# Performance work log

Measured on AMD Instinct MI355X. Metric: run time of the kernel, lower is better.

## Reference

```python
import jax, jax.numpy as jnp
import numpy as np

EMB = 1024
HEADS = 16
HEAD_DIM = EMB // HEADS
MASK_VAL = -10000.0


def setup_inputs() -> dict:
    key = jax.random.key(0)
    ks = jax.random.split(key, 5)
    B, S = 4, 2048
    x = jax.random.normal(ks[0], (B, S, EMB), dtype=jnp.float32)
    scale = 1.0 / np.sqrt(EMB)
    w_qkv = jax.random.normal(ks[1], (EMB, 3 * EMB), dtype=jnp.float32) * scale
    b_qkv = jnp.zeros((3 * EMB,), dtype=jnp.float32)
    w_fc = jax.random.normal(ks[2], (EMB, EMB), dtype=jnp.float32) * scale
    b_fc = jnp.zeros((EMB,), dtype=jnp.float32)
    return {"x": x, "w_qkv": w_qkv, "b_qkv": b_qkv, "w_fc": w_fc, "b_fc": b_fc}


def reference(x, w_qkv, b_qkv, w_fc, b_fc):
    B, S, _ = x.shape
    qkv = x @ w_qkv + b_qkv                      # (B, S, 3*EMB)
    q, k, v = jnp.split(qkv, 3, axis=-1)
    # split heads: (B, S, EMB) -> (B, H, S, Dh)
    def sh(t):
        return t.reshape(B, S, HEADS, HEAD_DIM).transpose(0, 2, 1, 3)
    q, k, v = sh(q), sh(k), sh(v)
    scores = jnp.einsum('bhqd,bhkd->bhqk', q, k) / np.sqrt(HEAD_DIM)
    causal = jnp.tril(jnp.ones((S, S), dtype=bool))[None, None]
    scores = jnp.where(causal, scores, jnp.float32(MASK_VAL))
    probs = jax.nn.softmax(scores, axis=-1)
    out = jnp.einsum('bhqk,bhkd->bhqd', probs, v)
    out = out.transpose(0, 2, 1, 3).reshape(B, S, EMB)  # merge heads
    return out @ w_fc + b_fc
```

## Files before the change

kernel.cpp:

```cpp
#include <hip/hip_runtime.h>
#include <hip/hip_bf16.h>
#include <cstdint>

#define BF16 __hip_bfloat16

typedef __attribute__((ext_vector_type(8))) short bhalf8;
typedef __attribute__((ext_vector_type(4))) float floatx4;

#define MFMA16(a, b, c) __builtin_amdgcn_mfma_f32_16x16x32_bf16((a), (b), (c), 0, 0, 0)

#define MASKV (-30000.0f)
#define QSCALE 0.18033688011112042f

__device__ __forceinline__ bhalf8 cvt8(const float* p) {
  const float4 f0 = *(const float4*)p;
  const float4 f1 = *(const float4*)(p + 4);
  union { bhalf8 v; ushort u[8]; } r;
  const float t[8] = {f0.x, f0.y, f0.z, f0.w, f1.x, f1.y, f1.z, f1.w};
#pragma unroll
  for (int i = 0; i < 8; ++i) {
    BF16 h = __float2bfloat16(t[i]);
    r.u[i] = *(const ushort*)&h;
  }
  return r.v;
}

__global__ void cvt_f32_bf16(const float* __restrict__ in, BF16* __restrict__ out) {
  const size_t i = ((size_t)blockIdx.x * 256 + threadIdx.x) * 8;
  *(bhalf8*)(out + i) = cvt8(in + i);
}

__global__ void transpose_cvt(const float* __restrict__ in, ushort* __restrict__ out,
                              int R, int C) {
  __shared__ ushort t[32][33];
  const int c0 = blockIdx.x * 32, r0 = blockIdx.y * 32;
  const int tx = threadIdx.x, ty = threadIdx.y;
#pragma unroll
  for (int j = 0; j < 32; j += 8) {
    BF16 h = __float2bfloat16(in[(size_t)(r0 + ty + j) * C + c0 + tx]);
    t[ty + j][tx] = *(const ushort*)&h;
  }
  __syncthreads();
#pragma unroll
  for (int j = 0; j < 32; j += 8)
    out[(size_t)(c0 + ty + j) * R + r0 + tx] = t[tx][ty + j];
}

template <int MODE>
__global__ __launch_bounds__(256, 2) void gemm_bt(
    const BF16* __restrict__ A, const BF16* __restrict__ Bt, const float* __restrict__ bias,
    void* __restrict__ C0v, BF16* __restrict__ C1, BF16* __restrict__ C2,
    int Md, int Nd, int Kd) {
  __shared__ __align__(16) BF16 As[128 * 64];
  __shared__ __align__(16) BF16 Bs[128 * 64];

  const int tid = threadIdx.x;
  const int w = tid >> 6, lane = tid & 63;
  const int lm = lane & 15, quad = lane >> 4;
  const int wm = (w >> 1) * 64, wn = (w & 1) * 64;
  const int tile_m = blockIdx.y * 128, tile_n = blockIdx.x * 128;

  floatx4 acc[4][4];
#pragma unroll
  for (int i = 0; i < 4; ++i)
#pragma unroll
    for (int j = 0; j < 4; ++j) acc[i][j] = (floatx4){0.f, 0.f, 0.f, 0.f};

  int srow[4], sgs[4], sslot[4];
#pragma unroll
  for (int j = 0; j < 4; ++j) {
    const int slot = (j * 4 + w) * 64 + lane;
    sslot[j] = slot;
    srow[j] = slot >> 3;
    sgs[j] = ((slot & 7) - (slot >> 3)) & 7;
  }

  bhalf8 va[4], vb[4], nva[4], nvb[4];
#pragma unroll
  for (int j = 0; j < 4; ++j) {
    va[j] = *(const bhalf8*)(A + (size_t)(tile_m + srow[j]) * Kd + sgs[j] * 8);
    vb[j] = *(const bhalf8*)(Bt + (size_t)(tile_n + srow[j]) * Kd + sgs[j] * 8);
  }

  for (int k0 = 0; k0 < Kd; k0 += 64) {
    __syncthreads();
#pragma unroll
    for (int j = 0; j < 4; ++j) {
      *(bhalf8*)(As + sslot[j] * 8) = va[j];
      *(bhalf8*)(Bs + sslot[j] * 8) = vb[j];
    }
    __syncthreads();

    if (k0 + 64 < Kd) {
      const int k1 = k0 + 64;
#pragma unroll
      for (int j = 0; j < 4; ++j) {
        nva[j] = *(const bhalf8*)(A + (size_t)(tile_m + srow[j]) * Kd + k1 + sgs[j] * 8);
        nvb[j] = *(const bhalf8*)(Bt + (size_t)(tile_n + srow[j]) * Kd + k1 + sgs[j] * 8);
      }
    }

#pragma unroll
    for (int s = 0; s < 2; ++s) {
      bhalf8 af[4], bfr[4];
#pragma unroll
      for (int mt = 0; mt < 4; ++mt) {
        const int r = wm + mt * 16 + lm;
        const int g = ((s * 4 + quad) + r) & 7;
        af[mt] = *(const bhalf8*)(As + r * 64 + g * 8);
      }
#pragma unroll
      for (int nt = 0; nt < 4; ++nt) {
        const int r = wn + nt * 16 + lm;
        const int g = ((s * 4 + quad) + r) & 7;
        bfr[nt] = *(const bhalf8*)(Bs + r * 64 + g * 8);
      }
#pragma unroll
      for (int mt = 0; mt < 4; ++mt)
#pragma unroll
        for (int nt = 0; nt < 4; ++nt)
          acc[mt][nt] = MFMA16(af[mt], bfr[nt], acc[mt][nt]);
    }
#pragma unroll
    for (int j = 0; j < 4; ++j) { va[j] = nva[j]; vb[j] = nvb[j]; }
  }

#pragma unroll
  for (int nt = 0; nt < 4; ++nt) {
    const int n = tile_n + wn + nt * 16 + lm;
    const float bv = bias[n];
#pragma unroll
    for (int mt = 0; mt < 4; ++mt) {
      const int m0 = tile_m + wm + mt * 16 + quad * 4;
      floatx4 v = acc[mt][nt];
      if (MODE == 0) {
        float* C0f = (float*)C0v;
#pragma unroll
        for (int r = 0; r < 4; ++r)
          C0f[(size_t)(m0 + r) * Nd + n] = v[r] + bv;
      } else {
        const int which = n >> 10;
        const int h = (n >> 6) & 15;
        const int d = n & 63;
        if (which == 2) {
          const int b = m0 >> 11, s0 = m0 & 2047;
          union { ushort4 u4; ushort u[4]; } pk;
#pragma unroll
          for (int r = 0; r < 4; ++r) {
            BF16 hv = __float2bfloat16(v[r] + bv);
            pk.u[r] = *(const ushort*)&hv;
          }
          *(ushort4*)(C2 + ((size_t)((b * 16 + h) * 64 + d)) * 2048 + s0) = pk.u4;
        } else {
          BF16* dst = (which == 0) ? (BF16*)C0v : C1;
          const float sc = (which == 0) ? QSCALE : 1.0f;
#pragma unroll
          for (int r = 0; r < 4; ++r) {
            const int m = m0 + r, b = m >> 11, si = m & 2047;
            dst[((size_t)(b * 16 + h) * 2048 + si) * 64 + d] =
                __float2bfloat16((v[r] + bv) * sc);
          }
        }
      }
    }
  }
}

__global__ __launch_bounds__(256, 2) void flash_attn(
    const BF16* __restrict__ Q, const BF16* __restrict__ Kmat,
    const BF16* __restrict__ VT, BF16* __restrict__ O) {
  __shared__ __align__(16) BF16 Ps[4][4][16 * 64];

  const int tid = threadIdx.x;
  const int w = tid >> 6, lane = tid & 63;
  const int lm = lane & 15, quad = lane >> 4;

  const int bid = blockIdx.x;
  const int xcd = bid & 7;
  const int li = bid >> 3;
  const int bh = xcd * 8 + (li >> 3);
  const int x = li & 7;

  const int qt = (w == 0) ? x : (w == 1) ? (15 - x) : (w == 2) ? (16 + x) : (31 - x);
  const int qb0 = qt * 64;
  const size_t bh_off = (size_t)bh * (2048 * 64);

  bhalf8 aq[4][2];
#pragma unroll
  for (int s2 = 0; s2 < 4; ++s2) {
    const BF16* qp = Q + bh_off + (size_t)(qb0 + s2 * 16 + lm) * 64 + quad * 8;
    aq[s2][0] = *(const bhalf8*)qp;
    aq[s2][1] = *(const bhalf8*)(qp + 32);
  }

  floatx4 oacc[4][4];
  float m_i[4], l_i[4];
#pragma unroll
  for (int s2 = 0; s2 < 4; ++s2) {
    m_i[s2] = MASKV;
    l_i[s2] = 0.f;
#pragma unroll
    for (int i = 0; i < 4; ++i) oacc[s2][i] = (floatx4){0.f, 0.f, 0.f, 0.f};
  }

  for (int kt = 0; kt <= qt; ++kt) {
    const int k0 = kt * 64;

    bhalf8 ak[4][2], av[4][2];
#pragma unroll
    for (int nt = 0; nt < 4; ++nt) {
      const BF16* kp = Kmat + bh_off + (size_t)(k0 + nt * 16 + lm) * 64 + quad * 8;
      ak[nt][0] = *(const bhalf8*)kp;
      ak[nt][1] = *(const bhalf8*)(kp + 32);
      const BF16* vp = VT + bh_off + (size_t)(nt * 16 + lm) * 2048 + k0 + quad * 8;
      av[nt][0] = *(const bhalf8*)vp;
      av[nt][1] = *(const bhalf8*)(vp + 32);
    }

#pragma unroll
    for (int s2 = 0; s2 < 4; ++s2) {
      const int qb = qb0 + s2 * 16;
      if (k0 > qb + 15) continue;

      floatx4 st[4];
#pragma unroll
      for (int nt = 0; nt < 4; ++nt) {
        floatx4 z = (floatx4){0.f, 0.f, 0.f, 0.f};
        z = MFMA16(ak[nt][0], aq[s2][0], z);
        z = MFMA16(ak[nt][1], aq[s2][1], z);
        st[nt] = z;
      }

      if (k0 + 63 > qb) {
#pragma unroll
        for (int nt = 0; nt < 4; ++nt)
#pragma unroll
          for (int r = 0; r < 4; ++r)
            if ((k0 + nt * 16 + quad * 4 + r) > (qb + lm)) st[nt][r] = MASKV;
      }

      float mx = MASKV;
#pragma unroll
      for (int nt = 0; nt < 4; ++nt)
#pragma unroll
        for (int r = 0; r < 4; ++r) mx = fmaxf(mx, st[nt][r]);
      mx = fmaxf(mx, __shfl_xor(mx, 16, 64));
      mx = fmaxf(mx, __shfl_xor(mx, 32, 64));

      if (!__all(mx <= m_i[s2] + 8.0f)) {
        const float mnew = fmaxf(m_i[s2], mx);
        const float alpha = __builtin_amdgcn_exp2f(m_i[s2] - mnew);
        m_i[s2] = mnew;
        l_i[s2] *= alpha;
#pragma unroll
        for (int dn = 0; dn < 4; ++dn) oacc[s2][dn] *= alpha;
      }

      float rs = 0.f;
#pragma unroll
      for (int nt = 0; nt < 4; ++nt)
#pragma unroll
        for (int r = 0; r < 4; ++r) {
          const float p = __builtin_amdgcn_exp2f(st[nt][r] - m_i[s2]);
          st[nt][r] = p;
          rs += p;
        }
      rs += __shfl_xor(rs, 16, 64);
      rs += __shfl_xor(rs, 32, 64);
      l_i[s2] += rs;

      BF16* pws = Ps[w][s2];
#pragma unroll
      for (int nt = 0; nt < 4; ++nt) {
        union { ushort4 u4; ushort u[4]; } pk;
#pragma unroll
        for (int r = 0; r < 4; ++r) {
          BF16 h = __float2bfloat16(st[nt][r]);
          pk.u[r] = *(const ushort*)&h;
        }
        const int g = ((nt * 2 + (quad >> 1)) + lm) & 7;
        *(ushort4*)(pws + lm * 64 + g * 8 + (quad & 1) * 4) = pk.u4;
      }

      const bhalf8 ap0 = *(const bhalf8*)(pws + lm * 64 + ((quad + lm) & 7) * 8);
      const bhalf8 ap1 = *(const bhalf8*)(pws + lm * 64 + ((4 + quad + lm) & 7) * 8);
#pragma unroll
      for (int dn = 0; dn < 4; ++dn) {
        oacc[s2][dn] = MFMA16(av[dn][0], ap0, oacc[s2][dn]);
        oacc[s2][dn] = MFMA16(av[dn][1], ap1, oacc[s2][dn]);
      }
    }
  }

  const int b = bh >> 4, h = bh & 15;
#pragma unroll
  for (int s2 = 0; s2 < 4; ++s2) {
    const float inv_l = 1.0f / l_i[s2];
    const size_t orow = (size_t)(b * 2048 + qb0 + s2 * 16 + lm) * 1024 + h * 64;
#pragma unroll
    for (int dn = 0; dn < 4; ++dn) {
      union { ushort4 u4; ushort u[4]; } pk;
#pragma unroll
      for (int r = 0; r < 4; ++r) {
        BF16 h2 = __float2bfloat16(oacc[s2][dn][r] * inv_l);
        pk.u[r] = *(const ushort*)&h2;
      }
      *(ushort4*)(O + orow + dn * 16 + quad * 4) = pk.u4;
    }
  }
}

extern "C" void kernel_launch(void* const* d_in, const int* in_sizes, int n_in,
                              void* d_out, int out_size, void* d_ws, size_t ws_size,
                              hipStream_t stream) {
  const float* x = (const float*)d_in[0];
  const float* w_qkv = (const float*)d_in[1];
  const float* b_qkv = (const float*)d_in[2];
  const float* w_fc = (const float*)d_in[3];
  const float* b_fc = (const float*)d_in[4];
  float* out = (float*)d_out;

  BF16* ws = (BF16*)d_ws;
  BF16* wTqkv = ws;
  BF16* wTfc = wTqkv + 3072 * 1024;
  BF16* xb = wTfc + 1024 * 1024;
  BF16* Qb = xb + 8388608;
  BF16* Kb = Qb + 8388608;
  BF16* VTb = Kb + 8388608;
  BF16* Ob = VTb + 8388608;

  cvt_f32_bf16<<<4096, 256, 0, stream>>>(x, xb);
  transpose_cvt<<<dim3(96, 32), dim3(32, 8), 0, stream>>>(w_qkv, (ushort*)wTqkv, 1024, 3072);
  transpose_cvt<<<dim3(32, 32), dim3(32, 8), 0, stream>>>(w_fc, (ushort*)wTfc, 1024, 1024);

  gemm_bt<1><<<dim3(24, 64), 256, 0, stream>>>(
      xb, wTqkv, b_qkv, (void*)Qb, Kb, VTb, 8192, 3072, 1024);
  flash_attn<<<dim3(512), 256, 0, stream>>>(Qb, Kb, VTb, Ob);
  gemm_bt<0><<<dim3(8, 64), 256, 0, stream>>>(
      Ob, wTfc, b_fc, (void*)out, nullptr, nullptr, 8192, 1024, 1024);
}
```

Baseline: 272.6 us.

## Software-pipeline PV MFMAs across sub-tiles, add setprio, and swizzle GEMM tile order

The attention inner loop now issues the PV MFMAs for the previous 16-row sub-tile after the softmax of the current one, so matrix work can overlap exp and LDS traffic. MFMA groups are wrapped in s_setprio to favour matrix issue. The skip for fully masked sub-tiles is removed, so those sub-tiles are now computed and rely on masking. The GEMM remaps block IDs with a stride-8 swizzle, likely to spread neighbouring tiles across XCDs or caches, and this assumes the block count divides by 8.

New measurement: 274.9 us. About the same (+0.8%).

```diff
diff --git a/kernel.cpp b/kernel.cpp
--- a/kernel.cpp
+++ b/kernel.cpp
@@ -58,7 +58,11 @@
   const int w = tid >> 6, lane = tid & 63;
   const int lm = lane & 15, quad = lane >> 4;
   const int wm = (w >> 1) * 64, wn = (w & 1) * 64;
-  const int tile_m = blockIdx.y * 128, tile_n = blockIdx.x * 128;
+
+  const int lin = blockIdx.y * gridDim.x + blockIdx.x;
+  const int per8 = (gridDim.x * gridDim.y) >> 3;
+  const int swz = (lin & 7) * per8 + (lin >> 3);
+  const int tile_m = (swz / gridDim.x) * 128, tile_n = (swz % gridDim.x) * 128;
 
   floatx4 acc[4][4];
 #pragma unroll
@@ -220,9 +224,9 @@
 #pragma unroll
     for (int s2 = 0; s2 < 4; ++s2) {
       const int qb = qb0 + s2 * 16;
-      if (k0 > qb + 15) continue;
 
       floatx4 st[4];
+      __builtin_amdgcn_s_setprio(1);
 #pragma unroll
       for (int nt = 0; nt < 4; ++nt) {
         floatx4 z = (floatx4){0.f, 0.f, 0.f, 0.f};
@@ -230,6 +234,7 @@
         z = MFMA16(ak[nt][1], aq[s2][1], z);
         st[nt] = z;
       }
+      __builtin_amdgcn_s_setprio(0);
 
       if (k0 + 63 > qb) {
 #pragma unroll
@@ -265,30 +270,52 @@
           st[nt][r] = p;
           rs += p;
         }
+
+      {
+        BF16* pws = Ps[w][s2];
+#pragma unroll
+        for (int nt = 0; nt < 4; ++nt) {
+          union { ushort4 u4; ushort u[4]; } pk;
+#pragma unroll
+          for (int r = 0; r < 4; ++r) {
+            BF16 h = __float2bfloat16(st[nt][r]);
+            pk.u[r] = *(const ushort*)&h;
+          }
+          const int g = ((nt * 2 + (quad >> 1)) + lm) & 7;
+          *(ushort4*)(pws + lm * 64 + g * 8 + (quad & 1) * 4) = pk.u4;
+        }
+      }
+
       rs += __shfl_xor(rs, 16, 64);
       rs += __shfl_xor(rs, 32, 64);
       l_i[s2] += rs;
 
-      BF16* pws = Ps[w][s2];
-#pragma unroll
-      for (int nt = 0; nt < 4; ++nt) {
-        union { ushort4 u4; ushort u[4]; } pk;
-#pragma unroll
-        for (int r = 0; r < 4; ++r) {
-          BF16 h = __float2bfloat16(st[nt][r]);
-          pk.u[r] = *(const ushort*)&h;
+      if (s2 > 0) {
+        const int sp = s2 - 1;
+        const BF16* pwp = Ps[w][sp];
+        const bhalf8 ap0 = *(const bhalf8*)(pwp + lm * 64 + ((quad + lm) & 7) * 8);
+        const bhalf8 ap1 = *(const bhalf8*)(pwp + lm * 64 + ((4 + quad + lm) & 7) * 8);
+        __builtin_amdgcn_s_setprio(1);
+#pragma unroll
+        for (int dn = 0; dn < 4; ++dn) {
+          oacc[sp][dn] = MFMA16(av[dn][0], ap0, oacc[sp][dn]);
+          oacc[sp][dn] = MFMA16(av[dn][1], ap1, oacc[sp][dn]);
         }
-        const int g = ((nt * 2 + (quad >> 1)) + lm) & 7;
-        *(ushort4*)(pws + lm * 64 + g * 8 + (quad & 1) * 4) = pk.u4;
-      }
-
-      const bhalf8 ap0 = *(const bhalf8*)(pws + lm * 64 + ((quad + lm) & 7) * 8);
-      const bhalf8 ap1 = *(const bhalf8*)(pws + lm * 64 + ((4 + quad + lm) & 7) * 8);
+        __builtin_amdgcn_s_setprio(0);
+      }
+    }
+
+    {
+      const BF16* pwp = Ps[w][3];
+      const bhalf8 ap0 = *(const bhalf8*)(pwp + lm * 64 + ((quad + lm) & 7) * 8);
+      const bhalf8 ap1 = *(const bhalf8*)(pwp + lm * 64 + ((4 + quad + lm) & 7) * 8);
+      __builtin_amdgcn_s_setprio(1);
 #pragma unroll
       for (int dn = 0; dn < 4; ++dn) {
-        oacc[s2][dn] = MFMA16(av[dn][0], ap0, oacc[s2][dn]);
-        oacc[s2][dn] = MFMA16(av[dn][1], ap1, oacc[s2][dn]);
-      }
+        oacc[3][dn] = MFMA16(av[dn][0], ap0, oacc[3][dn]);
+        oacc[3][dn] = MFMA16(av[dn][1], ap1, oacc[3][dn]);
+      }
+      __builtin_amdgcn_s_setprio(0);
     }
   }
 
```
